# Optimization experiments

Hardware: AMD Instinct MI355X
Metric: run time of the kernel (lower is better)

Reference implementation:

```python
import jax, jax.numpy as jnp
import numpy as np

EPS = 1e-7


def setup_inputs() -> dict:
    key = jax.random.key(0)
    k1, k2, k3, k4 = jax.random.split(key, 4)
    N, M = 8192, 8192
    inputs = jax.random.normal(k1, (N, 2), dtype=jnp.float32)
    outputs = jax.random.normal(k2, (N,), dtype=jnp.float32)
    x = jax.random.normal(k3, (M, 2), dtype=jnp.float32)
    # positive per-query bandwidths in [0.5, 1.5)
    bandwidth = 0.5 + jax.random.uniform(k4, (M,), dtype=jnp.float32)
    return {"x": x, "inputs": inputs, "outputs": outputs, "bandwidth": bandwidth}


def reference(x, inputs, outputs, bandwidth):
    # Squared pairwise distances (cdist followed by .pow(2) in the original):
    # d2[n, m] = ||inputs[n] - x[m]||^2, computed via the expansion to avoid
    # materializing an (N, M, 2) intermediate.
    a2 = jnp.sum(inputs * inputs, axis=1)  # (N,)
    b2 = jnp.sum(x * x, axis=1)            # (M,)
    d2 = a2[:, None] + b2[None, :] - 2.0 * (inputs @ x.T)  # (N, M)
    d2 = jnp.maximum(d2, 0.0)

    bw = bandwidth[None, :]  # (1, M), per-query bandwidth
    weights = jnp.exp(-d2 / (2.0 * bw * bw))  # (N, M)
    # Normalization over dim 0 (over the N reference points)
    weights = weights / (jnp.sum(weights, axis=0, keepdims=True) + EPS)
    # weights.T @ outputs -> (M,), Nadaraya-Watson weighted sum
    weighted = weights.T @ outputs  # (M,)
    return weighted
```

## Files before the change

### kernel.cpp

```cpp
#include <hip/hip_runtime.h>

#define EPS 1e-7f
#define LOG2E 1.44269504088896340736f

constexpr int SEGS  = 32;
constexpr int BLOCK = 256;

__global__ __launch_bounds__(BLOCK) void nw_partial(
    const float2* __restrict__ x,
    const float2* __restrict__ inputs,
    const float*  __restrict__ outputs,
    const float*  __restrict__ bw,
    float2*       __restrict__ partial,
    int N, int M)
{
    const int j   = blockIdx.x * BLOCK + threadIdx.x;
    const int seg = blockIdx.y;
    const int per = (N + SEGS - 1) / SEGS;
    const int i0  = seg * per;
    const int i1  = min(N, i0 + per);

    float x0 = 0.f, x1 = 0.f, k = 0.f;
    if (j < M) {
        float2 xj = x[j];
        x0 = xj.x;
        x1 = xj.y;
        float b = bw[j];
        k = -LOG2E / (2.0f * b * b);
    }

    float num = 0.f, den = 0.f;
    #pragma unroll 8
    for (int i = i0; i < i1; ++i) {
        float2 p  = inputs[i];
        float  oi = outputs[i];
        float dx = p.x - x0;
        float dy = p.y - x1;
        float d2 = fmaf(dx, dx, dy * dy);
        float w  = __builtin_amdgcn_exp2f(d2 * k);
        num = fmaf(w, oi, num);
        den += w;
    }

    if (j < M) partial[seg * M + j] = make_float2(num, den);
}

__global__ __launch_bounds__(BLOCK) void nw_finalize(
    const float2* __restrict__ partial,
    float*        __restrict__ out,
    int M)
{
    const int j = blockIdx.x * BLOCK + threadIdx.x;
    if (j >= M) return;
    float num = 0.f, den = 0.f;
    #pragma unroll
    for (int s = 0; s < SEGS; ++s) {
        float2 p = partial[s * M + j];
        num += p.x;
        den += p.y;
    }
    out[j] = num / (den + EPS);
}

extern "C" void kernel_launch(void* const* d_in, const int* in_sizes, int n_in,
                              void* d_out, int out_size, void* d_ws, size_t ws_size,
                              hipStream_t stream) {
    const float2* x       = (const float2*)d_in[0];
    const float2* inputs  = (const float2*)d_in[1];
    const float*  outputs = (const float*) d_in[2];
    const float*  bwv     = (const float*) d_in[3];
    const int N = in_sizes[2];
    const int M = in_sizes[3];
    float*        out     = (float*)d_out;
    float2*       partial = (float2*)d_ws;

    dim3 grid1((M + BLOCK - 1) / BLOCK, SEGS);
    nw_partial<<<grid1, BLOCK, 0, stream>>>(x, inputs, outputs, bwv, partial, N, M);

    dim3 grid2((M + BLOCK - 1) / BLOCK);
    nw_finalize<<<grid2, BLOCK, 0, stream>>>(partial, out, M);
}
```

Before: 79.85 us.

## Register-tile eight queries per thread and expand exponent into FMA form

Each thread now handles eight query points, reusing each loaded reference point and output value across them, and the segment count rises to keep the block count fixed. The exponent is precomputed as a quadratic in the reference point so each pair costs three FMAs before the exp2. This cuts per-pair load and ALU overhead, but enlarges the partial buffer and finalize reduction eightfold and adds cancellation risk from the expanded distance form.

Result: slower. 91.48 us (+14.6%).

```diff
diff --git a/kernel.cpp b/kernel.cpp
--- a/kernel.cpp
+++ b/kernel.cpp
@@ -3,8 +3,10 @@
 #define EPS 1e-7f
 #define LOG2E 1.44269504088896340736f
 
-constexpr int SEGS  = 32;
 constexpr int BLOCK = 256;
+constexpr int JT    = 8;
+constexpr int JBLK  = BLOCK * JT;
+constexpr int SEGS  = 256;
 
 __global__ __launch_bounds__(BLOCK) void nw_partial(
     const float2* __restrict__ x,
@@ -14,35 +16,52 @@
     float2*       __restrict__ partial,
     int N, int M)
 {
-    const int j   = blockIdx.x * BLOCK + threadIdx.x;
+    const int tid = threadIdx.x;
+    const int bx  = blockIdx.x;
     const int seg = blockIdx.y;
     const int per = (N + SEGS - 1) / SEGS;
     const int i0  = seg * per;
     const int i1  = min(N, i0 + per);
 
-    float x0 = 0.f, x1 = 0.f, k = 0.f;
-    if (j < M) {
-        float2 xj = x[j];
-        x0 = xj.x;
-        x1 = xj.y;
-        float b = bw[j];
-        k = -LOG2E / (2.0f * b * b);
+    float c0[JT], c1[JT], c2[JT], c3[JT], num[JT], den[JT];
+    #pragma unroll
+    for (int jt = 0; jt < JT; ++jt) {
+        const int j = bx * JBLK + jt * BLOCK + tid;
+        if (j < M) {
+            float2 xj = x[j];
+            float  b  = bw[j];
+            float  k  = -LOG2E / (2.0f * b * b);
+            c0[jt] = k;
+            c1[jt] = -2.0f * k * xj.x;
+            c2[jt] = -2.0f * k * xj.y;
+            c3[jt] = k * fmaf(xj.x, xj.x, xj.y * xj.y);
+        } else {
+            c0[jt] = c1[jt] = c2[jt] = 0.f;
+            c3[jt] = -1.0e38f;
+        }
+        num[jt] = 0.f;
+        den[jt] = 0.f;
     }
 
-    float num = 0.f, den = 0.f;
-    #pragma unroll 8
+    #pragma unroll 4
     for (int i = i0; i < i1; ++i) {
-        float2 p  = inputs[i];
-        float  oi = outputs[i];
-        float dx = p.x - x0;
-        float dy = p.y - x1;
-        float d2 = fmaf(dx, dx, dy * dy);
-        float w  = __builtin_amdgcn_exp2f(d2 * k);
-        num = fmaf(w, oi, num);
-        den += w;
+        float2 p = inputs[i];
+        float  o = outputs[i];
+        float  s = fmaf(p.x, p.x, p.y * p.y);
+        #pragma unroll
+        for (int jt = 0; jt < JT; ++jt) {
+            float t = fmaf(c0[jt], s, fmaf(c1[jt], p.x, fmaf(c2[jt], p.y, c3[jt])));
+            float w = __builtin_amdgcn_exp2f(t);
+            num[jt] = fmaf(w, o, num[jt]);
+            den[jt] += w;
+        }
     }
 
-    if (j < M) partial[seg * M + j] = make_float2(num, den);
+    #pragma unroll
+    for (int jt = 0; jt < JT; ++jt) {
+        const int j = bx * JBLK + jt * BLOCK + tid;
+        if (j < M) partial[(size_t)seg * M + j] = make_float2(num[jt], den[jt]);
+    }
 }
 
 __global__ __launch_bounds__(BLOCK) void nw_finalize(
@@ -53,9 +72,9 @@
     const int j = blockIdx.x * BLOCK + threadIdx.x;
     if (j >= M) return;
     float num = 0.f, den = 0.f;
-    #pragma unroll
+    #pragma unroll 8
     for (int s = 0; s < SEGS; ++s) {
-        float2 p = partial[s * M + j];
+        float2 p = partial[(size_t)s * M + j];
         num += p.x;
         den += p.y;
     }
@@ -74,9 +93,8 @@
     float*        out     = (float*)d_out;
     float2*       partial = (float2*)d_ws;
 
-    dim3 grid1((M + BLOCK - 1) / BLOCK, SEGS);
+    dim3 grid1((M + JBLK - 1) / JBLK, SEGS);
     nw_partial<<<grid1, BLOCK, 0, stream>>>(x, inputs, outputs, bwv, partial, N, M);
 
-    dim3 grid2((M + BLOCK - 1) / BLOCK);
-    nw_finalize<<<grid2, BLOCK, 0, stream>>>(partial, out, M);
+    nw_finalize<<<dim3((M + BLOCK - 1) / BLOCK), BLOCK, 0, stream>>>(partial, out, M);
 }
```
